# Performance work log

Measured on AMD Instinct MI355X. Metric: run time of the kernel, lower is better.

The kernel has to match this reference:

```python
import jax, jax.numpy as jnp
import numpy as np

B, T, C = 4, 2048, 1024
N_HEAD = 16
HEAD = C // N_HEAD

def setup_inputs() -> dict:
    key = jax.random.key(0)
    ks = jax.random.split(key, 5)
    return {
        "x": jax.random.normal(ks[0], (B, T, C), dtype=jnp.float32),
        "W_attn": jax.random.normal(ks[1], (C, 3 * C), dtype=jnp.float32) * (C ** -0.5),
        "b_attn": jax.random.normal(ks[2], (3 * C,), dtype=jnp.float32) * 0.02,
        "W_proj": jax.random.normal(ks[3], (C, C), dtype=jnp.float32) * (C ** -0.5),
        "b_proj": jax.random.normal(ks[4], (C,), dtype=jnp.float32) * 0.02,
    }

def reference(x, W_attn, b_attn, W_proj, b_proj):
    Bx, Tx, Cx = x.shape
    qkv = x @ W_attn + b_attn  # [B,T,3C]
    q, k, v = jnp.split(qkv, 3, axis=2)
    # [B,T,H,D] -> [B,H,T,D]
    q = q.reshape(Bx, Tx, N_HEAD, HEAD).transpose(0, 2, 1, 3)
    k = k.reshape(Bx, Tx, N_HEAD, HEAD).transpose(0, 2, 1, 3)
    v = v.reshape(Bx, Tx, N_HEAD, HEAD).transpose(0, 2, 1, 3)
    att = jnp.einsum('bhqd,bhkd->bhqk', q, k) * (HEAD ** -0.5)
    causal = jnp.tril(jnp.ones((Tx, Tx), dtype=bool))
    att = jnp.where(causal, att, jnp.float32(-jnp.inf))
    att = jax.nn.softmax(att, axis=-1)
    y = jnp.einsum('bhqk,bhkd->bhqd', att, v)
    y = y.transpose(0, 2, 1, 3).reshape(Bx, Tx, Cx)
    return y @ W_proj + b_proj
```

## Files before the change

### kernel.cpp

```cpp
#include <hip/hip_runtime.h>
#include <stdint.h>

#define NB 4
#define TT 2048
#define CC 1024
#define NH 16
#define DD 64
#define BHH (NB*NH)
#define MROWS (NB*TT)

typedef uint16_t u16;
typedef uint32_t u32;
typedef __bf16 bf16x8 __attribute__((ext_vector_type(8)));
typedef float f32x4 __attribute__((ext_vector_type(4)));
typedef float f32x16 __attribute__((ext_vector_type(16)));

__device__ __forceinline__ u16 f2bf(float f) {
    union { float f; uint32_t u; } v; v.f = f;
    uint32_t u = v.u;
    return (u16)((u + 0x7FFF + ((u >> 16) & 1)) >> 16);
}

__device__ __forceinline__ u32 cvtpk(float lo, float hi) {
    u32 r;
    asm volatile("v_cvt_pk_bf16_f32 %0, %1, %2" : "=v"(r) : "v"(lo), "v"(hi));
    return r;
}

__device__ __forceinline__ void plswap(u32& a, u32& b) {
    asm volatile("v_permlane32_swap_b32 %0, %1" : "+v"(a), "+v"(b));
}

__device__ __forceinline__ bf16x8 mk8(u32 a, u32 b, u32 c, u32 d) {
    union { u32 u[4]; bf16x8 v; } x;
    x.u[0] = a; x.u[1] = b; x.u[2] = c; x.u[3] = d;
    return x.v;
}

__device__ __forceinline__ void gl_lds16(const u16* g, u16* l) {
    __builtin_amdgcn_global_load_lds(
        (const __attribute__((address_space(1))) unsigned int*)g,
        (__attribute__((address_space(3))) unsigned int*)l, 16, 0, 0);
}

__device__ __forceinline__ f32x4 mfma16(bf16x8 a, bf16x8 b, f32x4 c) {
    return __builtin_amdgcn_mfma_f32_16x16x32_bf16(a, b, c, 0, 0, 0);
}
__device__ __forceinline__ f32x16 mfma32(bf16x8 a, bf16x8 b, f32x16 c) {
    return __builtin_amdgcn_mfma_f32_32x32x16_bf16(a, b, c, 0, 0, 0);
}

__global__ __launch_bounds__(256) void k_f2b(const float* __restrict__ in,
                                             u16* __restrict__ out, int n) {
    const int i = (blockIdx.x * 256 + threadIdx.x) * 4;
    if (i >= n) return;
    const float4 v = *(const float4*)(in + i);
    ushort4 o;
    o.x = f2bf(v.x); o.y = f2bf(v.y); o.z = f2bf(v.z); o.w = f2bf(v.w);
    *(ushort4*)(out + i) = o;
}

__global__ __launch_bounds__(256) void k_transpose_cvt(const float* __restrict__ in,
                                                       u16* __restrict__ out,
                                                       int R, int N) {
    __shared__ float t[32][33];
    const int n0 = blockIdx.x * 32, r0 = blockIdx.y * 32;
    const int c  = threadIdx.x & 31, rq = threadIdx.x >> 5;
#pragma unroll
    for (int i = 0; i < 4; ++i) {
        int r = rq + i * 8;
        t[r][c] = in[(r0 + r) * N + n0 + c];
    }
    __syncthreads();
#pragma unroll
    for (int i = 0; i < 4; ++i) {
        int r = rq + i * 8;
        out[(n0 + r) * R + r0 + c] = f2bf(t[c][r]);
    }
}

__device__ __forceinline__ void gemm128v2(const u16* __restrict__ A,
                                          const u16* __restrict__ Bt,
                                          int m0, int n0, f32x4 acc[4][4]) {
    __shared__ __align__(16) u16 As[2][128 * 64];
    __shared__ __align__(16) u16 Bs[2][128 * 64];
    const int tid = threadIdx.x, l = tid & 63, w = tid >> 6;
    const int wr = w >> 1, wc = w & 1;
    const int lr = l & 15, lg = l >> 4;

    auto stage = [&](int kt, int b) {
#pragma unroll
        for (int line = 0; line < 4; ++line) {
            const int s = line * 4096 + tid * 16;
            const int row = s >> 7;
            const int colb = (s & 127) ^ ((row & 7) << 4);
            const int ldsoff = (line * 4096 + w * 1024) >> 1;
            gl_lds16(A  + (size_t)(m0 + row) * 1024 + kt * 64 + (colb >> 1),
                     &As[b][ldsoff]);
            gl_lds16(Bt + (size_t)(n0 + row) * 1024 + kt * 64 + (colb >> 1),
                     &Bs[b][ldsoff]);
        }
    };

    stage(0, 0);
    __syncthreads();

    for (int kt = 0; kt < 16; ++kt) {
        const int b = kt & 1;
        if (kt < 15) stage(kt + 1, b ^ 1);
#pragma unroll
        for (int ks = 0; ks < 2; ++ks) {
            bf16x8 af[4], bf[4];
#pragma unroll
            for (int m = 0; m < 4; ++m) {
                const int row = wr * 64 + m * 16 + lr;
                const int byteC = (ks * 64 + lg * 16) ^ ((row & 7) << 4);
                af[m] = *(const bf16x8*)&As[b][(row * 128 + byteC) >> 1];
            }
#pragma unroll
            for (int n = 0; n < 4; ++n) {
                const int row = wc * 64 + n * 16 + lr;
                const int byteC = (ks * 64 + lg * 16) ^ ((row & 7) << 4);
                bf[n] = *(const bf16x8*)&Bs[b][(row * 128 + byteC) >> 1];
            }
#pragma unroll
            for (int m = 0; m < 4; ++m)
#pragma unroll
                for (int n = 0; n < 4; ++n)
                    acc[m][n] = mfma16(af[m], bf[n], acc[m][n]);
        }
        __syncthreads();
    }
}

__global__ __launch_bounds__(256, 2) void k_gemm_qkv(const u16* __restrict__ X,
                                                     const u16* __restrict__ Wt,
                                                     const float* __restrict__ bias,
                                                     u16* __restrict__ Qo,
                                                     u16* __restrict__ Ko,
                                                     u16* __restrict__ Vto) {
    const int id = blockIdx.x;
    const int xcd = id & 7, lid = id >> 3;
    const int lm = lid & 7, ln = lid >> 3;
    const int m0 = (xcd * 8 + lm) * 128;
    const int n0 = ln * 128;

    f32x4 acc[4][4];
#pragma unroll
    for (int m = 0; m < 4; ++m)
#pragma unroll
        for (int n = 0; n < 4; ++n) acc[m][n] = (f32x4){0.f, 0.f, 0.f, 0.f};
    gemm128v2(X, Wt, m0, n0, acc);

    const int tid = threadIdx.x, l = tid & 63, w = tid >> 6;
    const int wr = w >> 1, wc = w & 1, lr = l & 15, lg = l >> 4;
#pragma unroll
    for (int n = 0; n < 4; ++n) {
        const int c = n0 + wc * 64 + n * 16 + lr;
        const float bv = bias[c];
        const int which = c >> 10, cc = c & 1023, h = cc >> 6, d = cc & 63;
#pragma unroll
        for (int m = 0; m < 4; ++m) {
            const int rbase = m0 + wr * 64 + m * 16 + lg * 4;
#pragma unroll
            for (int j = 0; j < 4; ++j) {
                const int r = rbase + j;
                const int b = r >> 11, t = r & 2047;
                const int bh = b * NH + h;
                const u16 o = f2bf(acc[m][n][j] + bv);
                if (which == 0)      Qo[(bh * TT + t) * DD + d] = o;
                else if (which == 1) Ko[(bh * TT + t) * DD + d] = o;
                else                 Vto[(bh * DD + d) * TT + t] = o;
            }
        }
    }
}

__global__ __launch_bounds__(256, 2) void k_gemm_proj(const u16* __restrict__ Yin,
                                                      const u16* __restrict__ Wt,
                                                      const float* __restrict__ bias,
                                                      float* __restrict__ out) {
    const int id = blockIdx.x;
    const int xcd = id & 7, lid = id >> 3;
    const int lm = lid & 7, ln = lid >> 3;
    const int m0 = (xcd * 8 + lm) * 128;
    const int n0 = ln * 128;

    f32x4 acc[4][4];
#pragma unroll
    for (int m = 0; m < 4; ++m)
#pragma unroll
        for (int n = 0; n < 4; ++n) acc[m][n] = (f32x4){0.f, 0.f, 0.f, 0.f};
    gemm128v2(Yin, Wt, m0, n0, acc);

    const int tid = threadIdx.x, l = tid & 63, w = tid >> 6;
    const int wr = w >> 1, wc = w & 1, lr = l & 15, lg = l >> 4;
#pragma unroll
    for (int n = 0; n < 4; ++n) {
        const int c = n0 + wc * 64 + n * 16 + lr;
        const float bv = bias[c];
#pragma unroll
        for (int m = 0; m < 4; ++m) {
            const int rbase = m0 + wr * 64 + m * 16 + lg * 4;
#pragma unroll
            for (int j = 0; j < 4; ++j) {
                const int r = rbase + j;
                out[r * CC + c] = acc[m][n][j] + bv;
            }
        }
    }
}

__global__ __launch_bounds__(256) void k_attn(const u16* __restrict__ Qg_,
                                              const u16* __restrict__ Kg_,
                                              const u16* __restrict__ Vg_,
                                              u16* __restrict__ Y) {
    __shared__ __align__(16) u16 Ks[2][64 * 64];
    __shared__ __align__(16) u16 Vs[2][64 * 64];

    const int id = blockIdx.x;
    const int qi = 15 - (id >> 6);
    const int bh = id & 63;
    const int q0 = qi * 128;
    const u16* Qg = Qg_ + (size_t)bh * TT * DD;
    const u16* Kg = Kg_ + (size_t)bh * TT * DD;
    const u16* Vg = Vg_ + (size_t)bh * DD * TT;
    const int tid = threadIdx.x, l = tid & 63, w = tid >> 6;
    const int lq = l & 31, hi = l >> 5;
    const int qs = q0 + w * 32;

    unsigned dmask = 0;
#pragma unroll
    for (int r = 0; r < 16; ++r) {
        const int kvloc = (r & 3) + 8 * (r >> 2) + 4 * hi;
        if (kvloc > lq) dmask |= (1u << r);
    }

    const u16* qrow = Qg + (qs + lq) * DD + hi * 8;
    bf16x8 qf0 = *(const bf16x8*)(qrow);
    bf16x8 qf1 = *(const bf16x8*)(qrow + 16);
    bf16x8 qf2 = *(const bf16x8*)(qrow + 32);
    bf16x8 qf3 = *(const bf16x8*)(qrow + 48);

    f32x16 o0 = {}, o1 = {};
    float mrun = -1e30f, lrun = 0.f;
    const float C2 = 0.18033688011112042f;
    const int nt = 2 * qi + 2;

    auto stage = [&](int t, int b) {
        const int kv0 = t * 64;
#pragma unroll
        for (int iss = 0; iss < 2; ++iss) {
            const int s = iss * 4096 + tid * 16;
            const int row = s >> 7;
            const int colb = (s & 127) ^ ((row & 7) << 4);
            const int ldsoff = (iss * 4096 + w * 1024) >> 1;
            gl_lds16(Kg + (kv0 + row) * DD + (colb >> 1), &Ks[b][ldsoff]);
            gl_lds16(Vg + row * TT + kv0 + (colb >> 1),   &Vs[b][ldsoff]);
        }
    };

    stage(0, 0);
    __syncthreads();

    for (int t = 0; t < nt; ++t) {
        const int b = t & 1;
        if (t + 1 < nt) stage(t + 1, b ^ 1);
        const int kv0 = t * 64;

#pragma unroll
        for (int s = 0; s < 2; ++s) {
            const int kvs = kv0 + 32 * s;
            if (kvs > qs) continue;

            f32x16 st = {};
#pragma unroll
            for (int i = 0; i < 4; ++i) {
                const int row = 32 * s + lq;
                const int byte = (32 * i + 16 * hi) ^ ((row & 7) << 4);
                const bf16x8 kf = *(const bf16x8*)&Ks[b][(row * 128 + byte) >> 1];
                if (i == 0) st = mfma32(kf, qf0, st);
                else if (i == 1) st = mfma32(kf, qf1, st);
                else if (i == 2) st = mfma32(kf, qf2, st);
                else st = mfma32(kf, qf3, st);
            }

            if (kvs == qs) {
#pragma unroll
                for (int r = 0; r < 16; ++r)
                    if ((dmask >> r) & 1) st[r] = -1e30f;
            }

            float mx = st[0];
#pragma unroll
            for (int r = 1; r < 16; ++r) mx = fmaxf(mx, st[r]);
            mx = fmaxf(mx, __shfl_xor(mx, 32));

            if (!__all(mx <= mrun)) {
                const float mn = fmaxf(mrun, mx);
                const float scl = __builtin_amdgcn_exp2f((mrun - mn) * C2);
                mrun = mn;
                lrun *= scl;
#pragma unroll
                for (int r = 0; r < 16; ++r) { o0[r] *= scl; o1[r] *= scl; }
            }

            float psum = 0.f;
            u32 pk0, pk1, pk2, pk3, pk4, pk5, pk6, pk7;
            {
                float pa, pb;
                pa = __builtin_amdgcn_exp2f((st[0] - mrun) * C2);
                pb = __builtin_amdgcn_exp2f((st[1] - mrun) * C2);
                psum += pa + pb; pk0 = cvtpk(pa, pb);
                pa = __builtin_amdgcn_exp2f((st[2] - mrun) * C2);
                pb = __builtin_amdgcn_exp2f((st[3] - mrun) * C2);
                psum += pa + pb; pk1 = cvtpk(pa, pb);
                pa = __builtin_amdgcn_exp2f((st[4] - mrun) * C2);
                pb = __builtin_amdgcn_exp2f((st[5] - mrun) * C2);
                psum += pa + pb; pk2 = cvtpk(pa, pb);
                pa = __builtin_amdgcn_exp2f((st[6] - mrun) * C2);
                pb = __builtin_amdgcn_exp2f((st[7] - mrun) * C2);
                psum += pa + pb; pk3 = cvtpk(pa, pb);
                pa = __builtin_amdgcn_exp2f((st[8] - mrun) * C2);
                pb = __builtin_amdgcn_exp2f((st[9] - mrun) * C2);
                psum += pa + pb; pk4 = cvtpk(pa, pb);
                pa = __builtin_amdgcn_exp2f((st[10] - mrun) * C2);
                pb = __builtin_amdgcn_exp2f((st[11] - mrun) * C2);
                psum += pa + pb; pk5 = cvtpk(pa, pb);
                pa = __builtin_amdgcn_exp2f((st[12] - mrun) * C2);
                pb = __builtin_amdgcn_exp2f((st[13] - mrun) * C2);
                psum += pa + pb; pk6 = cvtpk(pa, pb);
                pa = __builtin_amdgcn_exp2f((st[14] - mrun) * C2);
                pb = __builtin_amdgcn_exp2f((st[15] - mrun) * C2);
                psum += pa + pb; pk7 = cvtpk(pa, pb);
            }
            lrun += psum;

            plswap(pk0, pk2); plswap(pk1, pk3);
            plswap(pk4, pk6); plswap(pk5, pk7);
            const bf16x8 pf0 = mk8(pk0, pk1, pk2, pk3);
            const bf16x8 pf1 = mk8(pk4, pk5, pk6, pk7);

#pragma unroll
            for (int dh = 0; dh < 2; ++dh) {
#pragma unroll
                for (int ks = 0; ks < 2; ++ks) {
                    const int row = 32 * dh + lq;
                    const int byte = (64 * s + 32 * ks + 16 * hi) ^ ((row & 7) << 4);
                    const bf16x8 vf = *(const bf16x8*)&Vs[b][(row * 128 + byte) >> 1];
                    if (dh == 0) o0 = mfma32(vf, ks ? pf1 : pf0, o0);
                    else         o1 = mfma32(vf, ks ? pf1 : pf0, o1);
                }
            }
        }
        if (t + 1 < nt) __syncthreads();
    }

    lrun += __shfl_xor(lrun, 32);
    const float inv = 1.0f / lrun;
    const int bb = bh >> 4, h = bh & 15;
    u16* yrow = Y + (size_t)(bb * TT + qs + lq) * CC + h * DD;
#pragma unroll
    for (int rq = 0; rq < 4; ++rq) {
        const int d0 = 8 * rq + 4 * hi;
        const u32 w0 = cvtpk(o0[rq * 4 + 0] * inv, o0[rq * 4 + 1] * inv);
        const u32 w1 = cvtpk(o0[rq * 4 + 2] * inv, o0[rq * 4 + 3] * inv);
        *(uint2*)&yrow[d0] = make_uint2(w0, w1);
        const u32 w2 = cvtpk(o1[rq * 4 + 0] * inv, o1[rq * 4 + 1] * inv);
        const u32 w3 = cvtpk(o1[rq * 4 + 2] * inv, o1[rq * 4 + 3] * inv);
        *(uint2*)&yrow[32 + d0] = make_uint2(w2, w3);
    }
}

extern "C" void kernel_launch(void* const* d_in, const int* in_sizes, int n_in,
                              void* d_out, int out_size, void* d_ws, size_t ws_size,
                              hipStream_t stream) {
    const float* X  = (const float*)d_in[0];
    const float* Wa = (const float*)d_in[1];
    const float* ba = (const float*)d_in[2];
    const float* Wp = (const float*)d_in[3];
    const float* bp = (const float*)d_in[4];
    float* out = (float*)d_out;

    u16* ws  = (u16*)d_ws;
    u16* Xb  = ws;
    u16* WtA = Xb + (size_t)MROWS * CC;
    u16* WtP = WtA + 3072 * 1024;
    u16* Qb  = WtP + 1024 * 1024;
    u16* Kb  = Qb + (size_t)BHH * TT * DD;
    u16* Vtb = Kb + (size_t)BHH * TT * DD;
    u16* Yb  = Vtb + (size_t)BHH * TT * DD;

    k_f2b<<<dim3(MROWS * CC / 1024), 256, 0, stream>>>(X, Xb, MROWS * CC);
    k_transpose_cvt<<<dim3(96, 32), 256, 0, stream>>>(Wa, WtA, 1024, 3072);
    k_transpose_cvt<<<dim3(32, 32), 256, 0, stream>>>(Wp, WtP, 1024, 1024);
    k_gemm_qkv<<<dim3(1536), 256, 0, stream>>>(Xb, WtA, ba, Qb, Kb, Vtb);
    k_attn<<<dim3(1024), 256, 0, stream>>>(Qb, Kb, Vtb, Yb);
    k_gemm_proj<<<dim3(512), 256, 0, stream>>>(Yb, WtP, bp, out);
}
```

Baseline: 188.3 us.

## Fold softmax scale into Q, compute row sums via MFMA, permute q-tile order

Multiplies Q by the softmax scale times log2(e) in the QKV epilogue, so the attention loop can apply exp2 directly without a per-element multiply. The row-sum accumulation moves from VALU adds and a cross-lane shuffle to two extra MFMAs against a ones vector, with the result read from the MFMA accumulator. The q-tile launch order is also permuted to interleave long and short causal tiles for better load balance. The risks are extra MFMA work per tile, a larger accumulator register footprint, and slightly different rounding because Q is scaled before the bf16 conversion.

```diff
diff --git a/kernel.cpp b/kernel.cpp
--- a/kernel.cpp
+++ b/kernel.cpp
@@ -152,6 +152,7 @@
         for (int n = 0; n < 4; ++n) acc[m][n] = (f32x4){0.f, 0.f, 0.f, 0.f};
     gemm128v2(X, Wt, m0, n0, acc);
 
+    const float C2 = 0.18033688011112042f;
     const int tid = threadIdx.x, l = tid & 63, w = tid >> 6;
     const int wr = w >> 1, wc = w & 1, lr = l & 15, lg = l >> 4;
 #pragma unroll
@@ -167,10 +168,10 @@
                 const int r = rbase + j;
                 const int b = r >> 11, t = r & 2047;
                 const int bh = b * NH + h;
-                const u16 o = f2bf(acc[m][n][j] + bv);
-                if (which == 0)      Qo[(bh * TT + t) * DD + d] = o;
-                else if (which == 1) Ko[(bh * TT + t) * DD + d] = o;
-                else                 Vto[(bh * DD + d) * TT + t] = o;
+                const float v = acc[m][n][j] + bv;
+                if (which == 0)      Qo[(bh * TT + t) * DD + d] = f2bf(v * C2);
+                else if (which == 1) Ko[(bh * TT + t) * DD + d] = f2bf(v);
+                else                 Vto[(bh * DD + d) * TT + t] = f2bf(v);
             }
         }
     }
@@ -219,7 +220,9 @@
     __shared__ __align__(16) u16 Vs[2][64 * 64];
 
     const int id = blockIdx.x;
-    const int qi = 15 - (id >> 6);
+    const int g = id >> 6;
+    const int qperm[16] = {15,14,13,12, 0,1,2,3, 11,10,9,8, 4,5,6,7};
+    const int qi = qperm[g];
     const int bh = id & 63;
     const int q0 = qi * 128;
     const u16* Qg = Qg_ + (size_t)bh * TT * DD;
@@ -242,9 +245,10 @@
     bf16x8 qf2 = *(const bf16x8*)(qrow + 32);
     bf16x8 qf3 = *(const bf16x8*)(qrow + 48);
 
-    f32x16 o0 = {}, o1 = {};
-    float mrun = -1e30f, lrun = 0.f;
-    const float C2 = 0.18033688011112042f;
+    const bf16x8 onesf = mk8(0x3F803F80u, 0x3F803F80u, 0x3F803F80u, 0x3F803F80u);
+
+    f32x16 o0 = {}, o1 = {}, lsum = {};
+    float mrun = -1e30f;
     const int nt = 2 * qi + 2;
 
     auto stage = [&](int t, int b) {
@@ -298,48 +302,49 @@
 
             if (!__all(mx <= mrun)) {
                 const float mn = fmaxf(mrun, mx);
-                const float scl = __builtin_amdgcn_exp2f((mrun - mn) * C2);
+                const float scl = __builtin_amdgcn_exp2f(mrun - mn);
                 mrun = mn;
-                lrun *= scl;
+                lsum[0] *= scl;
 #pragma unroll
                 for (int r = 0; r < 16; ++r) { o0[r] *= scl; o1[r] *= scl; }
             }
 
-            float psum = 0.f;
             u32 pk0, pk1, pk2, pk3, pk4, pk5, pk6, pk7;
             {
                 float pa, pb;
-                pa = __builtin_amdgcn_exp2f((st[0] - mrun) * C2);
-                pb = __builtin_amdgcn_exp2f((st[1] - mrun) * C2);
-                psum += pa + pb; pk0 = cvtpk(pa, pb);
-                pa = __builtin_amdgcn_exp2f((st[2] - mrun) * C2);
-                pb = __builtin_amdgcn_exp2f((st[3] - mrun) * C2);
-                psum += pa + pb; pk1 = cvtpk(pa, pb);
-                pa = __builtin_amdgcn_exp2f((st[4] - mrun) * C2);
-                pb = __builtin_amdgcn_exp2f((st[5] - mrun) * C2);
-                psum += pa + pb; pk2 = cvtpk(pa, pb);
-                pa = __builtin_amdgcn_exp2f((st[6] - mrun) * C2);
-                pb = __builtin_amdgcn_exp2f((st[7] - mrun) * C2);
-                psum += pa + pb; pk3 = cvtpk(pa, pb);
-                pa = __builtin_amdgcn_exp2f((st[8] - mrun) * C2);
-                pb = __builtin_amdgcn_exp2f((st[9] - mrun) * C2);
-                psum += pa + pb; pk4 = cvtpk(pa, pb);
-                pa = __builtin_amdgcn_exp2f((st[10] - mrun) * C2);
-                pb = __builtin_amdgcn_exp2f((st[11] - mrun) * C2);
-                psum += pa + pb; pk5 = cvtpk(pa, pb);
-                pa = __builtin_amdgcn_exp2f((st[12] - mrun) * C2);
-                pb = __builtin_amdgcn_exp2f((st[13] - mrun) * C2);
-                psum += pa + pb; pk6 = cvtpk(pa, pb);
-                pa = __builtin_amdgcn_exp2f((st[14] - mrun) * C2);
-                pb = __builtin_amdgcn_exp2f((st[15] - mrun) * C2);
-                psum += pa + pb; pk7 = cvtpk(pa, pb);
-            }
-            lrun += psum;
+                pa = __builtin_amdgcn_exp2f(st[0] - mrun);
+                pb = __builtin_amdgcn_exp2f(st[1] - mrun);
+                pk0 = cvtpk(pa, pb);
+                pa = __builtin_amdgcn_exp2f(st[2] - mrun);
+                pb = __builtin_amdgcn_exp2f(st[3] - mrun);
+                pk1 = cvtpk(pa, pb);
+                pa = __builtin_amdgcn_exp2f(st[4] - mrun);
+                pb = __builtin_amdgcn_exp2f(st[5] - mrun);
+                pk2 = cvtpk(pa, pb);
+                pa = __builtin_amdgcn_exp2f(st[6] - mrun);
+                pb = __builtin_amdgcn_exp2f(st[7] - mrun);
+                pk3 = cvtpk(pa, pb);
+                pa = __builtin_amdgcn_exp2f(st[8] - mrun);
+                pb = __builtin_amdgcn_exp2f(st[9] - mrun);
+                pk4 = cvtpk(pa, pb);
+                pa = __builtin_amdgcn_exp2f(st[10] - mrun);
+                pb = __builtin_amdgcn_exp2f(st[11] - mrun);
+                pk5 = cvtpk(pa, pb);
+                pa = __builtin_amdgcn_exp2f(st[12] - mrun);
+                pb = __builtin_amdgcn_exp2f(st[13] - mrun);
+                pk6 = cvtpk(pa, pb);
+                pa = __builtin_amdgcn_exp2f(st[14] - mrun);
+                pb = __builtin_amdgcn_exp2f(st[15] - mrun);
+                pk7 = cvtpk(pa, pb);
+            }
 
             plswap(pk0, pk2); plswap(pk1, pk3);
             plswap(pk4, pk6); plswap(pk5, pk7);
             const bf16x8 pf0 = mk8(pk0, pk1, pk2, pk3);
             const bf16x8 pf1 = mk8(pk4, pk5, pk6, pk7);
+
+            lsum = mfma32(onesf, pf0, lsum);
+            lsum = mfma32(onesf, pf1, lsum);
 
 #pragma unroll
             for (int dh = 0; dh < 2; ++dh) {
@@ -356,8 +361,7 @@
         if (t + 1 < nt) __syncthreads();
     }
 
-    lrun += __shfl_xor(lrun, 32);
-    const float inv = 1.0f / lrun;
+    const float inv = 1.0f / lsum[0];
     const int bb = bh >> 4, h = bh & 15;
     u16* yrow = Y + (size_t)(bb * TT + qs + lq) * CC + h * DD;
 #pragma unroll
```

Measured after the change: 209.6 us. +11.3%, slower.
